# Kernel optimization log

Measured on AMD Instinct MI355X. Metric: run time of the kernel, lower is better.

## Reference

```python
import jax, jax.numpy as jnp
import numpy as np

N = 50000      # nodes
E = 800000     # edges (avg degree 16)
F_IN = 256     # num_node_features
H = 256        # hidden_dim
L = 2          # num_message_passing_rounds - 1 hidden conv layers


def setup_inputs() -> dict:
    key = jax.random.key(0)
    ks = jax.random.split(key, 8)
    x = jax.random.normal(ks[0], (N, F_IN), dtype=jnp.float32)
    edge_index = jax.random.randint(ks[1], (2, E), 0, N, dtype=jnp.int32)
    init = lambda k, shape, fan: jax.random.normal(k, shape, dtype=jnp.float32) / np.float32(np.sqrt(fan))
    WA_in = init(ks[2], (F_IN, H), F_IN)   # proj_in.A weight (stored [in,out])
    WB_in = init(ks[3], (F_IN, H), F_IN)   # proj_in.B weight
    A_stack = init(ks[4], (L, H, H), H)    # conv layers' A weights
    B_stack = init(ks[5], (L, H, H), H)    # conv layers' B weights
    W_out = init(ks[6], (H, 1), H)         # proj_out weight
    b_out = jnp.zeros((1,), jnp.float32)   # proj_out bias
    return {"x": x, "edge_index": edge_index, "WA_in": WA_in, "WB_in": WB_in,
            "A_stack": A_stack, "B_stack": B_stack, "W_out": W_out, "b_out": b_out}


def reference(x, edge_index, WA_in, WB_in, A_stack, B_stack, W_out, b_out):
    src, dst = edge_index[0], edge_index[1]
    # in-degree per node; PyG scatter-mean divides by max(deg, 1)
    deg = jax.ops.segment_sum(jnp.ones((E,), x.dtype), dst, num_segments=N)
    inv_deg = (1.0 / jnp.maximum(deg, 1.0))[:, None]  # [N,1]

    def mean_agg(h):
        # gather x_j = h[src], scatter-mean into dst -> [N, d]
        return jax.ops.segment_sum(h[src], dst, num_segments=N) * inv_deg

    # proj_in: A(mean_msg) + B(x)
    h = mean_agg(x) @ WA_in + x @ WB_in
    # hidden conv rounds with sigmoid (use_relu=False)
    for i in range(L):
        h = jax.nn.sigmoid(mean_agg(h) @ A_stack[i] + h @ B_stack[i])
    # proj_out + squeeze (output_logits=True)
    return (h @ W_out + b_out).squeeze()  # [N]
```

## Files before the change

### kernel.cpp

```cpp
#include <hip/hip_runtime.h>

typedef unsigned char u8;
typedef unsigned short u16;
typedef unsigned int u32;
typedef __attribute__((ext_vector_type(8))) short short8;
typedef __attribute__((ext_vector_type(4))) float f32x4;
typedef __attribute__((ext_vector_type(2))) float f32x2;

__device__ __forceinline__ float bf2f(u16 u) {
    return __uint_as_float(((u32)u) << 16);
}
__device__ __forceinline__ u16 f2bf(float f) {
    u32 u = __float_as_uint(f);
    u += 0x7fff + ((u >> 16) & 1);
    return (u16)(u >> 16);
}
__device__ __forceinline__ u32 pack2(float a, float b) {
    return (u32)f2bf(a) | ((u32)f2bf(b) << 16);
}
__device__ __forceinline__ u32 pk_fp8x4(float f0, float f1, float f2, float f3) {
    int w = __builtin_amdgcn_cvt_pk_fp8_f32(f0, f1, 0, false);
    w = __builtin_amdgcn_cvt_pk_fp8_f32(f2, f3, w, true);
    return (u32)w;
}
__device__ __forceinline__ u8 f2fp8(float f) {
    return (u8)(__builtin_amdgcn_cvt_pk_fp8_f32(f, f, 0, false) & 0xff);
}
__device__ __forceinline__ void acc4(float* a, u32 w) {
    f32x2 lo = __builtin_amdgcn_cvt_pk_f32_fp8((int)w, false);
    f32x2 hi = __builtin_amdgcn_cvt_pk_f32_fp8((int)w, true);
    a[0] += lo.x; a[1] += lo.y; a[2] += hi.x; a[3] += hi.y;
}
__device__ __forceinline__ void acc4m(float* a, u32 w, float m) {
    f32x2 lo = __builtin_amdgcn_cvt_pk_f32_fp8((int)w, false);
    f32x2 hi = __builtin_amdgcn_cvt_pk_f32_fp8((int)w, true);
    a[0] += m * lo.x; a[1] += m * lo.y; a[2] += m * hi.x; a[3] += m * hi.y;
}
__device__ __forceinline__ void acc16(float* a, uint4 v) {
    acc4(a + 0, v.x); acc4(a + 4, v.y); acc4(a + 8, v.z); acc4(a + 12, v.w);
}
__device__ __forceinline__ void acc16m(float* a, uint4 v, float m) {
    acc4m(a + 0, v.x, m); acc4m(a + 4, v.y, m); acc4m(a + 8, v.z, m); acc4m(a + 12, v.w, m);
}


__global__ void cvt_x_kernel(const float* __restrict__ x, u16* __restrict__ xb,
                             u32* __restrict__ xq, int n) {
    int i = blockIdx.x * 256 + threadIdx.x;
    int row = i >> 6;
    ushort4 o;
    u32 q;
    if (row < n) {
        float4 v = ((const float4*)x)[i];
        o.x = f2bf(v.x); o.y = f2bf(v.y); o.z = f2bf(v.z); o.w = f2bf(v.w);
        q = pk_fp8x4(v.x, v.y, v.z, v.w);
    } else {
        o.x = o.y = o.z = o.w = 0;
        q = 0;
    }
    ((ushort4*)xb)[i] = o;
    xq[i] = q;
}

__global__ void cvt_w_kernel(const float* __restrict__ WA, const float* __restrict__ WB,
                             const float* __restrict__ As, const float* __restrict__ Bs,
                             u16* __restrict__ wT, int nlayers) {
    int i = blockIdx.x * 256 + threadIdx.x;
    const int per = 256 * 512;
    if (i >= nlayers * per) return;
    int l = i / per;
    int rem = i - l * per;
    int nn = rem >> 9;
    int k = rem & 511;
    const float* Aw = (l == 0) ? WA : As + (size_t)(l - 1) * 65536;
    const float* Bw = (l == 0) ? WB : Bs + (size_t)(l - 1) * 65536;
    float v = (k < 256) ? Aw[(size_t)k * 256 + nn] : Bw[(size_t)(k - 256) * 256 + nn];
    wT[i] = f2bf(v);
}


__global__ __launch_bounds__(256) void hist_kernel(const int* __restrict__ dst,
                                                   int* __restrict__ ccnt, int e, int nb) {
    __shared__ int h[256];
    int tid = threadIdx.x;
    h[tid] = 0;
    __syncthreads();
    int e0 = blockIdx.x * 4096;
#pragma unroll
    for (int j = 0; j < 16; ++j) {
        int i = e0 + j * 256 + tid;
        if (i < e) atomicAdd(&h[dst[i] >> 8], 1);
    }
    __syncthreads();
    if (tid < nb) {
        int v = h[tid];
        if (v) atomicAdd(&ccnt[tid], v);
    }
}

__global__ __launch_bounds__(256) void scan_coarse_kernel(const int* __restrict__ ccnt,
                                                          int* __restrict__ cbase,
                                                          int* __restrict__ rowptr,
                                                          int nb, int n, int e) {
    __shared__ int sh[256];
    int t = threadIdx.x;
    int v = (t < nb) ? ccnt[t] : 0;
    int x = v;
    sh[t] = x; __syncthreads();
    for (int o = 1; o < 256; o <<= 1) {
        int y = (t >= o) ? sh[t - o] : 0;
        __syncthreads();
        x += y; sh[t] = x; __syncthreads();
    }
    if (t < nb) cbase[t] = x - v;
    if (t == 0) { cbase[nb] = e; rowptr[n] = e; }
}

__global__ __launch_bounds__(256) void passA_kernel(const int* __restrict__ src,
                                                    const int* __restrict__ dst,
                                                    const int* __restrict__ cbase,
                                                    int* __restrict__ cfill,
                                                    u32* __restrict__ tmp, int e, int nb) {
    __shared__ int ph[256], pb[256], pr[256], cb[256];
    __shared__ u32 ed[4096];
    int tid = threadIdx.x;
    ph[tid] = 0; pr[tid] = 0;
    cb[tid] = (tid < nb) ? cbase[tid] : 0;
    __syncthreads();
    int e0 = blockIdx.x * 4096;
#pragma unroll
    for (int j = 0; j < 16; ++j) {
        int i = e0 + j * 256 + tid;
        u32 p = 0xFFFFFFFFu;
        if (i < e) {
            int d = dst[i];
            p = ((u32)d << 16) | (u32)src[i];
            atomicAdd(&ph[d >> 8], 1);
        }
        ed[j * 256 + tid] = p;
    }
    __syncthreads();
    pb[tid] = (tid < nb && ph[tid]) ? atomicAdd(&cfill[tid], ph[tid]) : 0;
    __syncthreads();
#pragma unroll
    for (int j = 0; j < 16; ++j) {
        u32 p = ed[j * 256 + tid];
        if (p != 0xFFFFFFFFu) {
            int bk = p >> 24;
            int r = atomicAdd(&pr[bk], 1);
            tmp[cb[bk] + pb[bk] + r] = p;
        }
    }
}

__global__ __launch_bounds__(256) void passB_kernel(const u32* __restrict__ tmp,
                                                    const int* __restrict__ cbase,
                                                    int* __restrict__ rowptr,
                                                    float* __restrict__ invd,
                                                    int* __restrict__ srcs, int n) {
    __shared__ int h[256], loc[256], cnt2[256], sh[256];
    int b = blockIdx.x;
    int tid = threadIdx.x;
    int base = cbase[b];
    int cnt = cbase[b + 1] - base;
    int node0 = b << 8;
    h[tid] = 0; cnt2[tid] = 0;
    __syncthreads();
    for (int i = tid; i < cnt; i += 256)
        atomicAdd(&h[(tmp[base + i] >> 16) & 255], 1);
    __syncthreads();
    int c = h[tid];
    int x = c;
    sh[tid] = x; __syncthreads();
    for (int o = 1; o < 256; o <<= 1) {
        int y = (tid >= o) ? sh[tid - o] : 0;
        __syncthreads();
        x += y; sh[tid] = x; __syncthreads();
    }
    loc[tid] = x - c;
    int node = node0 + tid;
    if (node < n) {
        rowptr[node] = base + x - c;
        invd[node] = 1.0f / (float)(c > 0 ? c : 1);
    }
    __syncthreads();
    for (int i = tid; i < cnt; i += 256) {
        u32 p = tmp[base + i];
        int ln = (p >> 16) & 255;
        int r = atomicAdd(&cnt2[ln], 1);
        srcs[base + loc[ln] + r] = (int)(p & 0xffffu);
    }
}


__global__ __launch_bounds__(256) void agg_kernel(const u8* __restrict__ q,
                                                  u16* __restrict__ mb,
                                                  const int* __restrict__ rowptr,
                                                  const int* __restrict__ srcs,
                                                  const float* __restrict__ invd,
                                                  int n, int npad) {
    int gw = (blockIdx.x * 256 + threadIdx.x) >> 6;
    int lane = threadIdx.x & 63;
    int qd = lane >> 4;
    int fl = lane & 15;
    if (gw >= npad) return;
    u16* orow = mb + (size_t)gw * 256;
    if (gw >= n) {
        if (lane < 16) {
            uint4 z; z.x = z.y = z.z = z.w = 0;
            uint4* p = (uint4*)(orow + lane * 16);
            p[0] = z; p[1] = z;
        }
        return;
    }
    int beg = rowptr[gw], end = rowptr[gw + 1];
    float a[16];
#pragma unroll
    for (int i = 0; i < 16; ++i) a[i] = 0.f;
    for (int base = beg; base < end; base += 64) {
        int cnt = end - base;
        if (cnt > 64) cnt = 64;
        int el = (lane < cnt) ? srcs[base + lane] : 0;
        int t = 0;
        for (; 4 * t + 8 <= cnt; t += 2) {
            int s0 = __shfl(el, 4 * t + qd);
            int s1 = __shfl(el, 4 * t + 4 + qd);
            uint4 v0 = *(const uint4*)(q + (size_t)s0 * 256 + fl * 16);
            uint4 v1 = *(const uint4*)(q + (size_t)s1 * 256 + fl * 16);
            acc16(a, v0);
            acc16(a, v1);
        }
        for (; 4 * t < cnt; ++t) {
            int ei = 4 * t + qd;
            int sj = __shfl(el, ei & 63);
            float m = (ei < cnt) ? 1.0f : 0.0f;
            uint4 v = *(const uint4*)(q + (size_t)sj * 256 + fl * 16);
            acc16m(a, v, m);
        }
    }
#pragma unroll
    for (int i = 0; i < 16; ++i) {
        a[i] += __shfl_xor(a[i], 16);
        a[i] += __shfl_xor(a[i], 32);
    }
    if (lane < 16) {
        float sc = invd[gw];
        uint4 o0, o1;
        o0.x = pack2(a[0] * sc, a[1] * sc);
        o0.y = pack2(a[2] * sc, a[3] * sc);
        o0.z = pack2(a[4] * sc, a[5] * sc);
        o0.w = pack2(a[6] * sc, a[7] * sc);
        o1.x = pack2(a[8] * sc, a[9] * sc);
        o1.y = pack2(a[10] * sc, a[11] * sc);
        o1.z = pack2(a[12] * sc, a[13] * sc);
        o1.w = pack2(a[14] * sc, a[15] * sc);
        uint4* p = (uint4*)(orow + lane * 16);
        p[0] = o0; p[1] = o1;
    }
}


__global__ __launch_bounds__(256) void gemm_kernel(const u16* __restrict__ mb,
                                                   const u16* __restrict__ cur,
                                                   const u16* __restrict__ wT,
                                                   u16* __restrict__ hout,
                                                   u8* __restrict__ hq,
                                                   const float* __restrict__ wo,
                                                   const float* __restrict__ bo,
                                                   float* __restrict__ out,
                                                   int n, int sig, int fin) {
    __shared__ u16 lA[8192];
    __shared__ u16 lB[8192];
    int tid = threadIdx.x;
    int bid = blockIdx.x;
    int ch = bid & 1;
    int r0 = (bid >> 1) * 128;
    int c0 = ch * 128;
    int lane = tid & 63;
    int w = tid >> 6;
    int wrow = w >> 1, wcol = w & 1;
    int lrow = lane & 15, quad = lane >> 4;

    f32x4 acc[4][4] = {};

    for (int ks = 0; ks < 8; ++ks) {
        const u16* sA = (ks < 4) ? mb : cur;
        int kk = (ks & 3) * 64;
        __syncthreads();
#pragma unroll
        for (int i = 0; i < 8; ++i) {
            int c = w * 8 + i;
            if (c < 16) {
                int s = c * 64 + lane;
                int row = s & 127, seg = s >> 7;
                const u16* g = sA + (size_t)(r0 + row) * 256 + kk + seg * 8;
                __builtin_amdgcn_global_load_lds(
                    (const __attribute__((address_space(1))) u32*)g,
                    (__attribute__((address_space(3))) u32*)(lA + (size_t)seg * 1024 + row * 8), 16, 0, 0);
            } else {
                int s = (c - 16) * 64 + lane;
                int row = s & 127, seg = s >> 7;
                const u16* g = wT + (size_t)(c0 + row) * 512 + ks * 64 + seg * 8;
                __builtin_amdgcn_global_load_lds(
                    (const __attribute__((address_space(1))) u32*)g,
                    (__attribute__((address_space(3))) u32*)(lB + (size_t)seg * 1024 + row * 8), 16, 0, 0);
            }
        }
        __syncthreads();

#pragma unroll
        for (int u = 0; u < 2; ++u) {
            short8 a[4], b[4];
#pragma unroll
            for (int rt = 0; rt < 4; ++rt) {
                int row = wrow * 64 + rt * 16 + lrow;
                a[rt] = *(const short8*)(lA + (size_t)(u * 4 + quad) * 1024 + row * 8);
            }
#pragma unroll
            for (int ct = 0; ct < 4; ++ct) {
                int col = wcol * 64 + ct * 16 + lrow;
                b[ct] = *(const short8*)(lB + (size_t)(u * 4 + quad) * 1024 + col * 8);
            }
#pragma unroll
            for (int rt = 0; rt < 4; ++rt)
#pragma unroll
                for (int ct = 0; ct < 4; ++ct)
                    acc[rt][ct] = __builtin_amdgcn_mfma_f32_16x16x32_bf16(a[rt], b[ct], acc[rt][ct], 0, 0, 0);
        }
    }

    if (!fin) {
#pragma unroll
        for (int rt = 0; rt < 4; ++rt) {
#pragma unroll
            for (int r = 0; r < 4; ++r) {
                int row = r0 + wrow * 64 + rt * 16 + quad * 4 + r;
#pragma unroll
                for (int ct = 0; ct < 4; ++ct) {
                    float v = acc[rt][ct][r];
                    if (sig) v = 1.0f / (1.0f + __expf(-v));
                    int col = c0 + wcol * 64 + ct * 16 + lrow;
                    hout[(size_t)row * 256 + col] = f2bf(v);
                    hq[(size_t)row * 256 + col] = f2fp8(v);
                }
            }
        }
    } else {
        float bo0 = bo[0];
        float wv[4];
#pragma unroll
        for (int ct = 0; ct < 4; ++ct) wv[ct] = wo[c0 + wcol * 64 + ct * 16 + lrow];
#pragma unroll
        for (int rt = 0; rt < 4; ++rt) {
#pragma unroll
            for (int r = 0; r < 4; ++r) {
                float s = 0.f;
#pragma unroll
                for (int ct = 0; ct < 4; ++ct) {
                    float v = acc[rt][ct][r];
                    v = 1.0f / (1.0f + __expf(-v));
                    s += v * wv[ct];
                }
                s += __shfl_xor(s, 1);
                s += __shfl_xor(s, 2);
                s += __shfl_xor(s, 4);
                s += __shfl_xor(s, 8);
                if (lrow == 0) {
                    int row = r0 + wrow * 64 + rt * 16 + quad * 4 + r;
                    if (row < n) atomicAdd(&out[row], s + ((ch == 0 && wcol == 0) ? bo0 : 0.f));
                }
            }
        }
    }
}


extern "C" void kernel_launch(void* const* d_in, const int* in_sizes, int n_in,
                              void* d_out, int out_size, void* d_ws, size_t ws_size,
                              hipStream_t stream) {
    const float* x  = (const float*)d_in[0];
    const int*   ei = (const int*)d_in[1];
    const float* WA = (const float*)d_in[2];
    const float* WB = (const float*)d_in[3];
    const float* As = (const float*)d_in[4];
    const float* Bs = (const float*)d_in[5];
    const float* Wo = (const float*)d_in[6];
    const float* bo = (const float*)d_in[7];
    float* out = (float*)d_out;

    const int H = 256;
    int N = in_sizes[0] / H;
    int E = in_sizes[1] / 2;
    int L = in_sizes[4] / (H * H);
    int NPAD = (N + 127) & ~127;
    int NB = (N + 255) >> 8;

    char* wsp = (char*)d_ws;
    size_t off = 0;
    auto alloc = [&](size_t b) { size_t o = off; off += (b + 255) & ~(size_t)255; return o; };
    int*   rowptr = (int*)(wsp + alloc((size_t)(NPAD + 1) * 4));
    int*   ccnt   = (int*)(wsp + alloc(1024));
    int*   cbase  = (int*)(wsp + alloc(1032 + 256));
    int*   cfill  = (int*)(wsp + alloc(1024));
    float* invd   = (float*)(wsp + alloc((size_t)NPAD * 4));
    int*   srcs   = (int*)(wsp + alloc((size_t)E * 4));
    u16*   xb     = (u16*)(wsp + alloc((size_t)NPAD * H * 2));
    u16*   h0     = (u16*)(wsp + alloc((size_t)NPAD * H * 2));
    u16*   h1     = (u16*)(wsp + alloc((size_t)NPAD * H * 2));
    u16*   mb     = (u16*)(wsp + alloc((size_t)NPAD * H * 2));
    u8*    xq     = (u8*)(wsp + alloc((size_t)NPAD * H));
    u8*    hq     = (u8*)(wsp + alloc((size_t)NPAD * H));
    u16*   wT     = (u16*)(wsp + alloc((size_t)(L + 1) * 512 * 256 * 2));
    u32*   tmp    = (u32*)mb;

    const int* esrc = ei;
    const int* edst = ei + E;

    hipMemsetAsync(ccnt, 0, 1024, stream);
    hipMemsetAsync(cfill, 0, 1024, stream);
    hipMemsetAsync(out, 0, (size_t)N * 4, stream);

    int gridE = (E + 4095) / 4096;
    cvt_x_kernel<<<NPAD / 4, 256, 0, stream>>>(x, xb, (u32*)xq, N);
    cvt_w_kernel<<<((L + 1) * 512 * 256 + 255) / 256, 256, 0, stream>>>(WA, WB, As, Bs, wT, L + 1);
    hist_kernel<<<gridE, 256, 0, stream>>>(edst, ccnt, E, NB);
    scan_coarse_kernel<<<1, 256, 0, stream>>>(ccnt, cbase, rowptr, NB, N, E);
    passA_kernel<<<gridE, 256, 0, stream>>>(esrc, edst, cbase, cfill, tmp, E, NB);
    passB_kernel<<<NB, 256, 0, stream>>>(tmp, cbase, rowptr, invd, srcs, N);

    const u16* cur = xb;
    const u8*  curq = xq;
    for (int s = 0; s <= L; ++s) {
        int fin = (s == L) ? 1 : 0;
        u16* nxt = (s & 1) ? h1 : h0;
        agg_kernel<<<NPAD / 4, 256, 0, stream>>>(curq, mb, rowptr, srcs, invd, N, NPAD);
        gemm_kernel<<<(NPAD / 128) * 2, 256, 0, stream>>>(mb, cur, wT + (size_t)s * 512 * 256,
                                                          nxt, hq, Wo, bo, out, N,
                                                          s > 0 ? 1 : 0, fin);
        if (!fin) {
            cur = nxt;
            curq = hq;
        }
    }
}
```

Before: 404.0 us.

## Transform before aggregating: GEMM h·[A|B] first, then gather projected features

Reorders each layer to compute h@A and h@B with a single GEMM over K=256 and N=512 outputs, storing h@A in fp8 and h@B in bf16. The aggregation kernel then gathers the projected fp8 rows, scales by inverse degree, adds h@B, applies the sigmoid, and either writes bf16 h or, in the final layer, fuses the output projection without atomics. The GEMM gains LDS double-buffering. This removes the concatenated-K GEMM, the separate fp8 copy of h and the output memset. The cost is a GB intermediate buffer, and because h@A is quantised to fp8 before the mean, the rounding error changes.

After: 395.0 us. 2.2% less time.

```diff
diff --git a/kernel.cpp b/kernel.cpp
--- a/kernel.cpp
+++ b/kernel.cpp
@@ -44,37 +44,32 @@
 }
 
 
-__global__ void cvt_x_kernel(const float* __restrict__ x, u16* __restrict__ xb,
-                             u32* __restrict__ xq, int n) {
+__global__ void cvt_x_kernel(const float* __restrict__ x, u16* __restrict__ xb, int n) {
     int i = blockIdx.x * 256 + threadIdx.x;
     int row = i >> 6;
     ushort4 o;
-    u32 q;
     if (row < n) {
         float4 v = ((const float4*)x)[i];
         o.x = f2bf(v.x); o.y = f2bf(v.y); o.z = f2bf(v.z); o.w = f2bf(v.w);
-        q = pk_fp8x4(v.x, v.y, v.z, v.w);
     } else {
         o.x = o.y = o.z = o.w = 0;
-        q = 0;
     }
     ((ushort4*)xb)[i] = o;
-    xq[i] = q;
 }
 
 __global__ void cvt_w_kernel(const float* __restrict__ WA, const float* __restrict__ WB,
                              const float* __restrict__ As, const float* __restrict__ Bs,
                              u16* __restrict__ wT, int nlayers) {
     int i = blockIdx.x * 256 + threadIdx.x;
-    const int per = 256 * 512;
+    const int per = 512 * 256;
     if (i >= nlayers * per) return;
     int l = i / per;
     int rem = i - l * per;
-    int nn = rem >> 9;
-    int k = rem & 511;
+    int nn = rem >> 8;
+    int k = rem & 255;
     const float* Aw = (l == 0) ? WA : As + (size_t)(l - 1) * 65536;
     const float* Bw = (l == 0) ? WB : Bs + (size_t)(l - 1) * 65536;
-    float v = (k < 256) ? Aw[(size_t)k * 256 + nn] : Bw[(size_t)(k - 256) * 256 + nn];
+    float v = (nn < 256) ? Aw[(size_t)k * 256 + nn] : Bw[(size_t)k * 256 + (nn - 256)];
     wT[i] = f2bf(v);
 }
 
@@ -193,22 +188,25 @@
 }
 
 
-__global__ __launch_bounds__(256) void agg_kernel(const u8* __restrict__ q,
-                                                  u16* __restrict__ mb,
+__global__ __launch_bounds__(256) void agg_kernel(const u8* __restrict__ GA,
+                                                  const u16* __restrict__ GB,
+                                                  u16* __restrict__ hout,
                                                   const int* __restrict__ rowptr,
                                                   const int* __restrict__ srcs,
                                                   const float* __restrict__ invd,
-                                                  int n, int npad) {
+                                                  const float* __restrict__ wo,
+                                                  const float* __restrict__ bo,
+                                                  float* __restrict__ out,
+                                                  int n, int npad, int sig, int fin) {
     int gw = (blockIdx.x * 256 + threadIdx.x) >> 6;
     int lane = threadIdx.x & 63;
     int qd = lane >> 4;
     int fl = lane & 15;
     if (gw >= npad) return;
-    u16* orow = mb + (size_t)gw * 256;
     if (gw >= n) {
-        if (lane < 16) {
+        if (!fin && lane < 16) {
             uint4 z; z.x = z.y = z.z = z.w = 0;
-            uint4* p = (uint4*)(orow + lane * 16);
+            uint4* p = (uint4*)(hout + (size_t)gw * 256 + lane * 16);
             p[0] = z; p[1] = z;
         }
         return;
@@ -225,8 +223,8 @@
         for (; 4 * t + 8 <= cnt; t += 2) {
             int s0 = __shfl(el, 4 * t + qd);
             int s1 = __shfl(el, 4 * t + 4 + qd);
-            uint4 v0 = *(const uint4*)(q + (size_t)s0 * 256 + fl * 16);
-            uint4 v1 = *(const uint4*)(q + (size_t)s1 * 256 + fl * 16);
+            uint4 v0 = *(const uint4*)(GA + (size_t)s0 * 256 + fl * 16);
+            uint4 v1 = *(const uint4*)(GA + (size_t)s1 * 256 + fl * 16);
             acc16(a, v0);
             acc16(a, v1);
         }
@@ -234,7 +232,7 @@
             int ei = 4 * t + qd;
             int sj = __shfl(el, ei & 63);
             float m = (ei < cnt) ? 1.0f : 0.0f;
-            uint4 v = *(const uint4*)(q + (size_t)sj * 256 + fl * 16);
+            uint4 v = *(const uint4*)(GA + (size_t)sj * 256 + fl * 16);
             acc16m(a, v, m);
         }
     }
@@ -245,91 +243,104 @@
     }
     if (lane < 16) {
         float sc = invd[gw];
-        uint4 o0, o1;
-        o0.x = pack2(a[0] * sc, a[1] * sc);
-        o0.y = pack2(a[2] * sc, a[3] * sc);
-        o0.z = pack2(a[4] * sc, a[5] * sc);
-        o0.w = pack2(a[6] * sc, a[7] * sc);
-        o1.x = pack2(a[8] * sc, a[9] * sc);
-        o1.y = pack2(a[10] * sc, a[11] * sc);
-        o1.z = pack2(a[12] * sc, a[13] * sc);
-        o1.w = pack2(a[14] * sc, a[15] * sc);
-        uint4* p = (uint4*)(orow + lane * 16);
-        p[0] = o0; p[1] = o1;
-    }
-}
-
-
-__global__ __launch_bounds__(256) void gemm_kernel(const u16* __restrict__ mb,
-                                                   const u16* __restrict__ cur,
+        const u16* gb = GB + (size_t)gw * 256 + lane * 16;
+        uint4 g0 = ((const uint4*)gb)[0];
+        uint4 g1 = ((const uint4*)gb)[1];
+        u32 gp[8] = {g0.x, g0.y, g0.z, g0.w, g1.x, g1.y, g1.z, g1.w};
+        float v[16];
+#pragma unroll
+        for (int j = 0; j < 8; ++j) {
+            v[2 * j]     = a[2 * j] * sc     + bf2f(gp[j] & 0xffff);
+            v[2 * j + 1] = a[2 * j + 1] * sc + bf2f(gp[j] >> 16);
+        }
+        if (sig) {
+#pragma unroll
+            for (int i = 0; i < 16; ++i) v[i] = 1.0f / (1.0f + __expf(-v[i]));
+        }
+        if (!fin) {
+            uint4 o0, o1;
+            o0.x = pack2(v[0], v[1]);   o0.y = pack2(v[2], v[3]);
+            o0.z = pack2(v[4], v[5]);   o0.w = pack2(v[6], v[7]);
+            o1.x = pack2(v[8], v[9]);   o1.y = pack2(v[10], v[11]);
+            o1.z = pack2(v[12], v[13]); o1.w = pack2(v[14], v[15]);
+            uint4* p = (uint4*)(hout + (size_t)gw * 256 + lane * 16);
+            p[0] = o0; p[1] = o1;
+        } else {
+            const float4* wv = (const float4*)(wo + lane * 16);
+            float s = 0.f;
+#pragma unroll
+            for (int j = 0; j < 4; ++j) {
+                float4 wf = wv[j];
+                s += v[4 * j] * wf.x + v[4 * j + 1] * wf.y +
+                     v[4 * j + 2] * wf.z + v[4 * j + 3] * wf.w;
+            }
+            s += __shfl_xor(s, 1);
+            s += __shfl_xor(s, 2);
+            s += __shfl_xor(s, 4);
+            s += __shfl_xor(s, 8);
+            if (lane == 0) out[gw] = s + bo[0];
+        }
+    }
+}
+
+
+__global__ __launch_bounds__(256) void gemm_kernel(const u16* __restrict__ hsrc,
                                                    const u16* __restrict__ wT,
-                                                   u16* __restrict__ hout,
-                                                   u8* __restrict__ hq,
-                                                   const float* __restrict__ wo,
-                                                   const float* __restrict__ bo,
-                                                   float* __restrict__ out,
-                                                   int n, int sig, int fin) {
-    __shared__ u16 lA[8192];
-    __shared__ u16 lB[8192];
+                                                   u8* __restrict__ GA,
+                                                   u16* __restrict__ GB) {
+    __shared__ u16 lA[2][4096];
+    __shared__ u16 lB[2][4096];
     int tid = threadIdx.x;
     int bid = blockIdx.x;
-    int ch = bid & 1;
-    int r0 = (bid >> 1) * 128;
-    int c0 = ch * 128;
+    int cq = bid & 3;
+    int r0 = (bid >> 2) << 7;
+    int c0 = cq << 7;
     int lane = tid & 63;
     int w = tid >> 6;
     int wrow = w >> 1, wcol = w & 1;
     int lrow = lane & 15, quad = lane >> 4;
 
+    auto stage = [&](int ks, int b) {
+#pragma unroll
+        for (int i = 0; i < 2; ++i) {
+            int s = (w * 2 + i) * 64 + lane;
+            int row = s & 127, seg = s >> 7;
+            const u16* g = hsrc + (size_t)(r0 + row) * 256 + ks * 32 + seg * 8;
+            __builtin_amdgcn_global_load_lds(
+                (const __attribute__((address_space(1))) u32*)g,
+                (__attribute__((address_space(3))) u32*)(&lA[b][(size_t)seg * 1024 + row * 8]), 16, 0, 0);
+            const u16* g2 = wT + (size_t)(c0 + row) * 256 + ks * 32 + seg * 8;
+            __builtin_amdgcn_global_load_lds(
+                (const __attribute__((address_space(1))) u32*)g2,
+                (__attribute__((address_space(3))) u32*)(&lB[b][(size_t)seg * 1024 + row * 8]), 16, 0, 0);
+        }
+    };
+
     f32x4 acc[4][4] = {};
-
+    stage(0, 0);
     for (int ks = 0; ks < 8; ++ks) {
-        const u16* sA = (ks < 4) ? mb : cur;
-        int kk = (ks & 3) * 64;
         __syncthreads();
-#pragma unroll
-        for (int i = 0; i < 8; ++i) {
-            int c = w * 8 + i;
-            if (c < 16) {
-                int s = c * 64 + lane;
-                int row = s & 127, seg = s >> 7;
-                const u16* g = sA + (size_t)(r0 + row) * 256 + kk + seg * 8;
-                __builtin_amdgcn_global_load_lds(
-                    (const __attribute__((address_space(1))) u32*)g,
-                    (__attribute__((address_space(3))) u32*)(lA + (size_t)seg * 1024 + row * 8), 16, 0, 0);
-            } else {
-                int s = (c - 16) * 64 + lane;
-                int row = s & 127, seg = s >> 7;
-                const u16* g = wT + (size_t)(c0 + row) * 512 + ks * 64 + seg * 8;
-                __builtin_amdgcn_global_load_lds(
-                    (const __attribute__((address_space(1))) u32*)g,
-                    (__attribute__((address_space(3))) u32*)(lB + (size_t)seg * 1024 + row * 8), 16, 0, 0);
-            }
-        }
-        __syncthreads();
-
-#pragma unroll
-        for (int u = 0; u < 2; ++u) {
-            short8 a[4], b[4];
-#pragma unroll
-            for (int rt = 0; rt < 4; ++rt) {
-                int row = wrow * 64 + rt * 16 + lrow;
-                a[rt] = *(const short8*)(lA + (size_t)(u * 4 + quad) * 1024 + row * 8);
-            }
-#pragma unroll
-            for (int ct = 0; ct < 4; ++ct) {
-                int col = wcol * 64 + ct * 16 + lrow;
-                b[ct] = *(const short8*)(lB + (size_t)(u * 4 + quad) * 1024 + col * 8);
-            }
-#pragma unroll
-            for (int rt = 0; rt < 4; ++rt)
-#pragma unroll
-                for (int ct = 0; ct < 4; ++ct)
-                    acc[rt][ct] = __builtin_amdgcn_mfma_f32_16x16x32_bf16(a[rt], b[ct], acc[rt][ct], 0, 0, 0);
-        }
-    }
-
-    if (!fin) {
+        if (ks < 7) stage(ks + 1, (ks + 1) & 1);
+        int buf = ks & 1;
+        short8 a[4], b[4];
+#pragma unroll
+        for (int rt = 0; rt < 4; ++rt) {
+            int row = wrow * 64 + rt * 16 + lrow;
+            a[rt] = *(const short8*)(&lA[buf][(size_t)quad * 1024 + row * 8]);
+        }
+#pragma unroll
+        for (int ct = 0; ct < 4; ++ct) {
+            int col = wcol * 64 + ct * 16 + lrow;
+            b[ct] = *(const short8*)(&lB[buf][(size_t)quad * 1024 + col * 8]);
+        }
+#pragma unroll
+        for (int rt = 0; rt < 4; ++rt)
+#pragma unroll
+            for (int ct = 0; ct < 4; ++ct)
+                acc[rt][ct] = __builtin_amdgcn_mfma_f32_16x16x32_bf16(a[rt], b[ct], acc[rt][ct], 0, 0, 0);
+    }
+
+    if (c0 < 256) {
 #pragma unroll
         for (int rt = 0; rt < 4; ++rt) {
 #pragma unroll
@@ -337,37 +348,22 @@
                 int row = r0 + wrow * 64 + rt * 16 + quad * 4 + r;
 #pragma unroll
                 for (int ct = 0; ct < 4; ++ct) {
-                    float v = acc[rt][ct][r];
-                    if (sig) v = 1.0f / (1.0f + __expf(-v));
                     int col = c0 + wcol * 64 + ct * 16 + lrow;
-                    hout[(size_t)row * 256 + col] = f2bf(v);
-                    hq[(size_t)row * 256 + col] = f2fp8(v);
+                    GA[(size_t)row * 256 + col] = f2fp8(acc[rt][ct][r]);
                 }
             }
         }
     } else {
-        float bo0 = bo[0];
-        float wv[4];
-#pragma unroll
-        for (int ct = 0; ct < 4; ++ct) wv[ct] = wo[c0 + wcol * 64 + ct * 16 + lrow];
+        int cb = c0 - 256;
 #pragma unroll
         for (int rt = 0; rt < 4; ++rt) {
 #pragma unroll
             for (int r = 0; r < 4; ++r) {
-                float s = 0.f;
+                int row = r0 + wrow * 64 + rt * 16 + quad * 4 + r;
 #pragma unroll
                 for (int ct = 0; ct < 4; ++ct) {
-                    float v = acc[rt][ct][r];
-                    v = 1.0f / (1.0f + __expf(-v));
-                    s += v * wv[ct];
-                }
-                s += __shfl_xor(s, 1);
-                s += __shfl_xor(s, 2);
-                s += __shfl_xor(s, 4);
-                s += __shfl_xor(s, 8);
-                if (lrow == 0) {
-                    int row = r0 + wrow * 64 + rt * 16 + quad * 4 + r;
-                    if (row < n) atomicAdd(&out[row], s + ((ch == 0 && wcol == 0) ? bo0 : 0.f));
+                    int col = cb + wcol * 64 + ct * 16 + lrow;
+                    GB[(size_t)row * 256 + col] = f2bf(acc[rt][ct][r]);
                 }
             }
         }
@@ -405,23 +401,21 @@
     float* invd   = (float*)(wsp + alloc((size_t)NPAD * 4));
     int*   srcs   = (int*)(wsp + alloc((size_t)E * 4));
     u16*   xb     = (u16*)(wsp + alloc((size_t)NPAD * H * 2));
-    u16*   h0     = (u16*)(wsp + alloc((size_t)NPAD * H * 2));
     u16*   h1     = (u16*)(wsp + alloc((size_t)NPAD * H * 2));
-    u16*   mb     = (u16*)(wsp + alloc((size_t)NPAD * H * 2));
-    u8*    xq     = (u8*)(wsp + alloc((size_t)NPAD * H));
-    u8*    hq     = (u8*)(wsp + alloc((size_t)NPAD * H));
+    u16*   h2     = (u16*)(wsp + alloc((size_t)NPAD * H * 2));
+    u8*    GA     = (u8*)(wsp + alloc((size_t)NPAD * H));
+    u16*   GB     = (u16*)(wsp + alloc((size_t)NPAD * H * 2));
     u16*   wT     = (u16*)(wsp + alloc((size_t)(L + 1) * 512 * 256 * 2));
-    u32*   tmp    = (u32*)mb;
+    u32*   tmp    = (u32*)GA;
 
     const int* esrc = ei;
     const int* edst = ei + E;
 
     hipMemsetAsync(ccnt, 0, 1024, stream);
     hipMemsetAsync(cfill, 0, 1024, stream);
-    hipMemsetAsync(out, 0, (size_t)N * 4, stream);
 
     int gridE = (E + 4095) / 4096;
-    cvt_x_kernel<<<NPAD / 4, 256, 0, stream>>>(x, xb, (u32*)xq, N);
+    cvt_x_kernel<<<NPAD / 4, 256, 0, stream>>>(x, xb, N);
     cvt_w_kernel<<<((L + 1) * 512 * 256 + 255) / 256, 256, 0, stream>>>(WA, WB, As, Bs, wT, L + 1);
     hist_kernel<<<gridE, 256, 0, stream>>>(edst, ccnt, E, NB);
     scan_coarse_kernel<<<1, 256, 0, stream>>>(ccnt, cbase, rowptr, NB, N, E);
@@ -429,17 +423,13 @@
     passB_kernel<<<NB, 256, 0, stream>>>(tmp, cbase, rowptr, invd, srcs, N);
 
     const u16* cur = xb;
-    const u8*  curq = xq;
     for (int s = 0; s <= L; ++s) {
         int fin = (s == L) ? 1 : 0;
-        u16* nxt = (s & 1) ? h1 : h0;
-        agg_kernel<<<NPAD / 4, 256, 0, stream>>>(curq, mb, rowptr, srcs, invd, N, NPAD);
-        gemm_kernel<<<(NPAD / 128) * 2, 256, 0, stream>>>(mb, cur, wT + (size_t)s * 512 * 256,
-                                                          nxt, hq, Wo, bo, out, N,
-                                                          s > 0 ? 1 : 0, fin);
-        if (!fin) {
-            cur = nxt;
-            curq = hq;
-        }
-    }
-}
+        int sig = (s > 0) ? 1 : 0;
+        u16* nxt = (s & 1) ? h2 : h1;
+        gemm_kernel<<<(NPAD / 128) * 4, 256, 0, stream>>>(cur, wT + (size_t)s * 512 * 256, GA, GB);
+        agg_kernel<<<NPAD / 4, 256, 0, stream>>>(GA, GB, nxt, rowptr, srcs, invd,
+                                                 Wo, bo, out, N, NPAD, sig, fin);
+        cur = nxt;
+    }
+}
```
